# Kernel tuning notes

Measured on AMD Instinct MI355X. Metric: run time of the kernel, lower is better.

Reference implementation:

```python
import jax, jax.numpy as jnp
import numpy as np

E = 1024
H = 16
DH = E // H
FF = 4096
EPS = 1e-5


def setup_inputs() -> dict:
    key = jax.random.key(0)
    ks = jax.random.split(key, 16)
    s = 1.0 / np.sqrt(E)
    sf = 1.0 / np.sqrt(FF)
    inp = {
        'x': jax.random.normal(ks[0], (4, 2048, E), dtype=jnp.float32),
        'Wq': jax.random.uniform(ks[1], (E, E), minval=-s, maxval=s, dtype=jnp.float32),
        'bq': jnp.zeros((E,), jnp.float32),
        'Wk': jax.random.uniform(ks[2], (E, E), minval=-s, maxval=s, dtype=jnp.float32),
        'bk': jnp.zeros((E,), jnp.float32),
        'Wv': jax.random.uniform(ks[3], (E, E), minval=-s, maxval=s, dtype=jnp.float32),
        'bv': jnp.zeros((E,), jnp.float32),
        'Wo': jax.random.uniform(ks[4], (E, E), minval=-s, maxval=s, dtype=jnp.float32),
        'bo': jnp.zeros((E,), jnp.float32),
        'W1': jax.random.uniform(ks[5], (E, FF), minval=-s, maxval=s, dtype=jnp.float32),
        'b1': jnp.zeros((FF,), jnp.float32),
        'W2': jax.random.uniform(ks[6], (FF, E), minval=-sf, maxval=sf, dtype=jnp.float32),
        'b2': jnp.zeros((E,), jnp.float32),
        'g1': jnp.ones((E,), jnp.float32),
        'be1': jnp.zeros((E,), jnp.float32),
        'g2': jnp.ones((E,), jnp.float32),
        'be2': jnp.zeros((E,), jnp.float32),
    }
    return inp


def _layernorm(x, g, b):
    mu = jnp.mean(x, axis=-1, keepdims=True)
    var = jnp.mean(jnp.square(x - mu), axis=-1, keepdims=True)
    return (x - mu) * jax.lax.rsqrt(var + EPS) * g + b


def reference(x, Wq, bq, Wk, bk, Wv, bv, Wo, bo, W1, b1, W2, b2, g1, be1, g2, be2):
    N, S, _ = x.shape
    # project and split heads: (N, H, S, DH)
    def heads(W, b):
        return (x @ W + b).reshape(N, S, H, DH).transpose(0, 2, 1, 3)
    q, k, v = heads(Wq, bq), heads(Wk, bk), heads(Wv, bv)
    scores = jnp.einsum('nhsd,nhtd->nhst', q, k) / np.sqrt(DH)
    attn = jax.nn.softmax(scores, axis=-1)
    ctx = jnp.einsum('nhst,nhtd->nhsd', attn, v)
    ctx = ctx.transpose(0, 2, 1, 3).reshape(N, S, H * DH)
    mh = ctx @ Wo + bo
    norm = _layernorm(mh + x, g1, be1)
    ff = jax.nn.relu(norm @ W1 + b1) @ W2 + b2
    return _layernorm(ff + norm, g2, be2)
```

## Files before the change

### kernel.cpp

```cpp
#include <hip/hip_runtime.h>
#include <hip/hip_bf16.h>
#include <math.h>

#define E_    1024
#define H_    16
#define DH_   64
#define FF_   4096
#define S_    2048
#define NB_   4
#define NTOK_ 8192

typedef float          f32x4_t  __attribute__((ext_vector_type(4)));
typedef unsigned short u16x8_t  __attribute__((ext_vector_type(8)));
typedef unsigned short u16x4_t  __attribute__((ext_vector_type(4)));
typedef __bf16         bf16x8_t __attribute__((ext_vector_type(8)));

#define BC8(x) __builtin_bit_cast(bf16x8_t, (x))

static __device__ __forceinline__ unsigned short f2bf(float f) {
  unsigned u = __float_as_uint(f);
  return (unsigned short)((u + 0x7FFF + ((u >> 16) & 1)) >> 16);
}

static __device__ __forceinline__ void gl16(const unsigned short* g, unsigned short* l) {
  __builtin_amdgcn_global_load_lds((const __attribute__((address_space(1))) void*)g,
                                   (__attribute__((address_space(3))) void*)l, 16, 0, 0);
}

__global__ __launch_bounds__(256)
void cvt_bf16_k(const float* __restrict__ in, unsigned short* __restrict__ out)
{
  const size_t i = ((size_t)blockIdx.x * 256 + threadIdx.x) * 4;
  const float4 v = *(const float4*)&in[i];
  u16x4_t p;
  p[0] = f2bf(v.x); p[1] = f2bf(v.y); p[2] = f2bf(v.z); p[3] = f2bf(v.w);
  *(u16x4_t*)&out[i] = p;
}

__global__ __launch_bounds__(256)
void transpose_bf16_k(const float* __restrict__ W,
                      unsigned short* __restrict__ Th, int K, int N)
{
  __shared__ float tile[64][65];
  const int t  = threadIdx.x;
  const int n0 = blockIdx.x * 64;
  const int k0 = blockIdx.y * 64;
#pragma unroll
  for (int i = 0; i < 4; ++i) {
    const int idx = t + 256 * i;
    const int r  = idx >> 4;
    const int c4 = (idx & 15) * 4;
    const float4 v = *(const float4*)&W[(size_t)(k0 + r) * N + n0 + c4];
    tile[r][c4 + 0] = v.x; tile[r][c4 + 1] = v.y;
    tile[r][c4 + 2] = v.z; tile[r][c4 + 3] = v.w;
  }
  __syncthreads();
#pragma unroll
  for (int i = 0; i < 4; ++i) {
    const int idx = t + 256 * i;
    const int rr  = idx >> 4;
    const int c4  = (idx & 15) * 4;
    u16x4_t hv;
#pragma unroll
    for (int j = 0; j < 4; ++j) hv[j] = f2bf(tile[c4 + j][rr]);
    *(u16x4_t*)&Th[(size_t)(n0 + rr) * K + k0 + c4] = hv;
  }
}

template<int RELU, int MODE>
__global__ __launch_bounds__(256)
void gemm_bf16_k(const unsigned short* __restrict__ A,
                 const unsigned short* __restrict__ Th,
                 const float* __restrict__ bias, void* __restrict__ outp,
                 int M, int N, int K)
{
  __shared__ __align__(16) unsigned short As[128][64];
  __shared__ __align__(16) unsigned short Bs[128][64];
  const int t    = threadIdx.x;
  const int nwg  = gridDim.x * gridDim.y;
  int id = blockIdx.x + gridDim.x * blockIdx.y;
  id = (id & 7) * (nwg >> 3) + (id >> 3);
  const int bn = (id % gridDim.x) * 128;
  const int bm = (id / gridDim.x) * 128;
  const int lane = t & 63;
  const int wid  = t >> 6;
  const int wr   = wid >> 1;
  const int wc   = wid & 1;
  const int fr   = lane & 15;
  const int hi   = lane >> 4;

  const int r8  = lane >> 3;
  const int csw = (lane & 7) ^ r8;

  f32x4_t acc[4][4];
#pragma unroll
  for (int m = 0; m < 4; ++m)
#pragma unroll
    for (int n = 0; n < 4; ++n)
#pragma unroll
      for (int j = 0; j < 4; ++j) acc[m][n][j] = 0.0f;

  const unsigned short* agl = A  + (size_t)(bm + wid * 32 + r8) * K + csw * 8;
  const unsigned short* bgl = Th + (size_t)(bn + wid * 32 + r8) * K + csw * 8;
  unsigned short* al = &As[wid * 32][0];
  unsigned short* bl = &Bs[wid * 32][0];

  for (int k0 = 0; k0 < K; k0 += 64) {
    __syncthreads();
#pragma unroll
    for (int i = 0; i < 4; ++i) {
      gl16(agl + (size_t)(i * 8) * K + k0, al + i * 512);
      gl16(bgl + (size_t)(i * 8) * K + k0, bl + i * 512);
    }
    __syncthreads();
#pragma unroll
    for (int kk = 0; kk < 2; ++kk) {
      u16x8_t aH[4], bH[4];
#pragma unroll
      for (int m = 0; m < 4; ++m)
        aH[m] = *(const u16x8_t*)&As[wr * 64 + m * 16 + fr][(((kk << 2) | hi) ^ (fr & 7)) * 8];
#pragma unroll
      for (int n = 0; n < 4; ++n)
        bH[n] = *(const u16x8_t*)&Bs[wc * 64 + n * 16 + fr][(((kk << 2) | hi) ^ (fr & 7)) * 8];
#pragma unroll
      for (int m = 0; m < 4; ++m)
#pragma unroll
        for (int n = 0; n < 4; ++n)
          acc[m][n] = __builtin_amdgcn_mfma_f32_16x16x32_bf16(BC8(aH[m]), BC8(bH[n]), acc[m][n], 0, 0, 0);
    }
  }

#pragma unroll
  for (int n = 0; n < 4; ++n) {
    const int col = bn + wc * 64 + n * 16 + fr;
    const float bv = bias[col];
#pragma unroll
    for (int m = 0; m < 4; ++m) {
      const int row0 = bm + wr * 64 + m * 16 + hi * 4;
      if (MODE == 2) {
        const int nb = row0 >> 11;
        const int s  = row0 & 2047;
        const int hh = col >> 6;
        const int dd = col & 63;
        u16x4_t pk;
#pragma unroll
        for (int j = 0; j < 4; ++j) pk[j] = f2bf(acc[m][n][j] + bv);
        *(u16x4_t*)&((unsigned short*)outp)[((size_t)((nb * H_ + hh) * DH_ + dd)) * S_ + s] = pk;
      } else {
#pragma unroll
        for (int j = 0; j < 4; ++j) {
          float v = acc[m][n][j] + bv;
          if (RELU) v = fmaxf(v, 0.0f);
          const size_t o = (size_t)(row0 + j) * N + col;
          if (MODE == 0) ((float*)outp)[o] = v;
          else           ((unsigned short*)outp)[o] = f2bf(v);
        }
      }
    }
  }
}

__global__ __launch_bounds__(256)
void attn_mfma_k(const unsigned short* __restrict__ Qg,
                 const unsigned short* __restrict__ Kg,
                 const unsigned short* __restrict__ VTg,
                 unsigned short* __restrict__ Og)
{
  __shared__ __align__(16) unsigned short Ks[64][72];
  __shared__ __align__(16) unsigned short Vt[64][72];
  __shared__ __align__(16) unsigned short Ps[128][72];

  const int t = threadIdx.x;
  const int nwg = gridDim.x * gridDim.y * gridDim.z;
  int id = blockIdx.x + gridDim.x * (blockIdx.y + gridDim.y * blockIdx.z);
  id = (id & 7) * (nwg >> 3) + (id >> 3);
  const int qt = id & 15;
  const int h  = (id >> 4) & 15;
  const int n  = id >> 8;

  const int lane = t & 63;
  const int wid  = t >> 6;
  const int fr   = lane & 15;
  const int hi   = lane >> 4;
  const size_t baseq = (size_t)n * S_ * E_ + (size_t)h * DH_;
  const size_t basev = (size_t)(n * H_ + h) * DH_ * S_;

  u16x8_t qv[2][2];
#pragma unroll
  for (int qf = 0; qf < 2; ++qf)
#pragma unroll
    for (int kk = 0; kk < 2; ++kk)
      qv[qf][kk] = *(const u16x8_t*)&Qg[baseq + (size_t)(qt * 128 + wid * 32 + qf * 16 + fr) * E_ + kk * 32 + hi * 8];

  f32x4_t acc[2][4];
  float m_run[2], l_run[2];
#pragma unroll
  for (int m = 0; m < 2; ++m) {
    m_run[m] = -INFINITY; l_run[m] = 0.0f;
#pragma unroll
    for (int nn = 0; nn < 4; ++nn)
#pragma unroll
      for (int j = 0; j < 4; ++j) acc[m][nn][j] = 0.0f;
  }

  const float cs = 0.18033688011112042f;

  for (int kt = 0; kt < S_ / 64; ++kt) {
    u16x8_t kr[2], vr[2];
#pragma unroll
    for (int i = 0; i < 2; ++i) {
      const int idx = t + 256 * i;
      const int r   = idx >> 3;
      const int c8  = (idx & 7) * 8;
      kr[i] = *(const u16x8_t*)&Kg[baseq + (size_t)(kt * 64 + r) * E_ + c8];
      vr[i] = *(const u16x8_t*)&VTg[basev + (size_t)r * S_ + kt * 64 + c8];
    }
    __syncthreads();
#pragma unroll
    for (int i = 0; i < 2; ++i) {
      const int idx = t + 256 * i;
      const int r   = idx >> 3;
      const int c8  = (idx & 7) * 8;
      *(u16x8_t*)&Ks[r][c8] = kr[i];
      *(u16x8_t*)&Vt[r][c8] = vr[i];
    }
    __syncthreads();

    f32x4_t s[4][2];
#pragma unroll
    for (int kf = 0; kf < 4; ++kf)
#pragma unroll
      for (int qf = 0; qf < 2; ++qf)
#pragma unroll
        for (int j = 0; j < 4; ++j) s[kf][qf][j] = 0.0f;
#pragma unroll
    for (int kk = 0; kk < 2; ++kk) {
      u16x8_t ak[4];
#pragma unroll
      for (int kf = 0; kf < 4; ++kf)
        ak[kf] = *(const u16x8_t*)&Ks[kf * 16 + fr][kk * 32 + hi * 8];
#pragma unroll
      for (int kf = 0; kf < 4; ++kf)
#pragma unroll
        for (int qf = 0; qf < 2; ++qf)
          s[kf][qf] = __builtin_amdgcn_mfma_f32_16x16x32_bf16(BC8(ak[kf]), BC8(qv[qf][kk]), s[kf][qf], 0, 0, 0);
    }

    float corrs[2];
#pragma unroll
    for (int qf = 0; qf < 2; ++qf) {
      float pm = s[0][qf][0];
#pragma unroll
      for (int kf = 0; kf < 4; ++kf)
#pragma unroll
        for (int j = 0; j < 4; ++j) pm = fmaxf(pm, s[kf][qf][j]);
      pm *= cs;
      pm = fmaxf(pm, __shfl_xor(pm, 16));
      pm = fmaxf(pm, __shfl_xor(pm, 32));
      const float mn   = fmaxf(m_run[qf], pm);
      const float corr = exp2f(m_run[qf] - mn);
      float ps = 0.0f;
#pragma unroll
      for (int kf = 0; kf < 4; ++kf)
#pragma unroll
        for (int j = 0; j < 4; ++j) {
          const float pv = exp2f(s[kf][qf][j] * cs - mn);
          Ps[wid * 32 + qf * 16 + fr][kf * 16 + hi * 4 + j] = f2bf(pv);
          ps += pv;
        }
      ps += __shfl_xor(ps, 16);
      ps += __shfl_xor(ps, 32);
      l_run[qf] = l_run[qf] * corr + ps;
      m_run[qf] = mn;
      corrs[qf] = corr;
    }

#pragma unroll
    for (int m = 0; m < 2; ++m)
#pragma unroll
      for (int j = 0; j < 4; ++j) {
        const float ca = __shfl(corrs[m], hi * 20 + j);
#pragma unroll
        for (int nn = 0; nn < 4; ++nn) acc[m][nn][j] *= ca;
      }

    asm volatile("s_waitcnt lgkmcnt(0)" ::: "memory");

#pragma unroll
    for (int kk = 0; kk < 2; ++kk) {
      u16x8_t ap[2], bv[4];
#pragma unroll
      for (int m = 0; m < 2; ++m)
        ap[m] = *(const u16x8_t*)&Ps[wid * 32 + m * 16 + fr][kk * 32 + hi * 8];
#pragma unroll
      for (int nn = 0; nn < 4; ++nn)
        bv[nn] = *(const u16x8_t*)&Vt[nn * 16 + fr][kk * 32 + hi * 8];
#pragma unroll
      for (int m = 0; m < 2; ++m)
#pragma unroll
        for (int nn = 0; nn < 4; ++nn)
          acc[m][nn] = __builtin_amdgcn_mfma_f32_16x16x32_bf16(BC8(ap[m]), BC8(bv[nn]), acc[m][nn], 0, 0, 0);
    }
  }

#pragma unroll
  for (int m = 0; m < 2; ++m)
#pragma unroll
    for (int j = 0; j < 4; ++j) {
      const float inv = 1.0f / __shfl(l_run[m], hi * 20 + j);
      const size_t o = baseq + (size_t)(qt * 128 + wid * 32 + m * 16 + hi * 4 + j) * E_;
#pragma unroll
      for (int nn = 0; nn < 4; ++nn)
        Og[o + nn * 16 + fr] = f2bf(acc[m][nn][j] * inv);
    }
}

template<int WB16>
__global__ __launch_bounds__(256)
void add_ln_k(const float* __restrict__ A, const float* __restrict__ B,
              const float* __restrict__ g, const float* __restrict__ be,
              float* __restrict__ out, unsigned short* __restrict__ outb)
{
  __shared__ float red[8];
  const int row = blockIdx.x;
  const int t = threadIdx.x;
  const size_t off = (size_t)row * E_ + t * 4;
  const float4 a = *(const float4*)&A[off];
  const float4 b = *(const float4*)&B[off];
  float4 x;
  x.x = a.x + b.x; x.y = a.y + b.y; x.z = a.z + b.z; x.w = a.w + b.w;

  float s = x.x + x.y + x.z + x.w;
  s += __shfl_xor(s, 1);  s += __shfl_xor(s, 2);  s += __shfl_xor(s, 4);
  s += __shfl_xor(s, 8);  s += __shfl_xor(s, 16); s += __shfl_xor(s, 32);
  if ((t & 63) == 0) red[t >> 6] = s;
  __syncthreads();
  const float mu = (red[0] + red[1] + red[2] + red[3]) * (1.0f / E_);

  float4 xc;
  xc.x = x.x - mu; xc.y = x.y - mu; xc.z = x.z - mu; xc.w = x.w - mu;
  float q = xc.x*xc.x + xc.y*xc.y + xc.z*xc.z + xc.w*xc.w;
  q += __shfl_xor(q, 1);  q += __shfl_xor(q, 2);  q += __shfl_xor(q, 4);
  q += __shfl_xor(q, 8);  q += __shfl_xor(q, 16); q += __shfl_xor(q, 32);
  __syncthreads();
  if ((t & 63) == 0) red[4 + (t >> 6)] = q;
  __syncthreads();
  const float var = (red[4] + red[5] + red[6] + red[7]) * (1.0f / E_);
  const float inv = rsqrtf(var + 1e-5f);

  const float4 gg = *(const float4*)&g[t * 4];
  const float4 bb = *(const float4*)&be[t * 4];
  float4 o;
  o.x = xc.x * inv * gg.x + bb.x;
  o.y = xc.y * inv * gg.y + bb.y;
  o.z = xc.z * inv * gg.z + bb.z;
  o.w = xc.w * inv * gg.w + bb.w;
  *(float4*)&out[off] = o;
  if (WB16) {
    u16x4_t p;
    p[0] = f2bf(o.x); p[1] = f2bf(o.y); p[2] = f2bf(o.z); p[3] = f2bf(o.w);
    *(u16x4_t*)&outb[off] = p;
  }
}

extern "C" void kernel_launch(void* const* d_in, const int* in_sizes, int n_in,
                              void* d_out, int out_size, void* d_ws, size_t ws_size,
                              hipStream_t stream)
{
  const float* x   = (const float*)d_in[0];
  const float* Wq  = (const float*)d_in[1];
  const float* bq  = (const float*)d_in[2];
  const float* Wk  = (const float*)d_in[3];
  const float* bk  = (const float*)d_in[4];
  const float* Wv  = (const float*)d_in[5];
  const float* bv  = (const float*)d_in[6];
  const float* Wo  = (const float*)d_in[7];
  const float* bo  = (const float*)d_in[8];
  const float* W1  = (const float*)d_in[9];
  const float* b1  = (const float*)d_in[10];
  const float* W2  = (const float*)d_in[11];
  const float* b2  = (const float*)d_in[12];
  const float* g1  = (const float*)d_in[13];
  const float* be1 = (const float*)d_in[14];
  const float* g2  = (const float*)d_in[15];
  const float* be2 = (const float*)d_in[16];
  float* out = (float*)d_out;
  char* wsb  = (char*)d_ws;

  const size_t MB = 1ull << 20;
  unsigned short* xb  = (unsigned short*)(wsb);
  unsigned short* Cb  = (unsigned short*)(wsb);
  unsigned short* Qb  = (unsigned short*)(wsb + 16 * MB);
  unsigned short* Kb  = (unsigned short*)(wsb + 32 * MB);
  unsigned short* F1  = (unsigned short*)(wsb);
  float*          Mh  = (float*)         (wsb + 16 * MB);
  unsigned short* VT  = (unsigned short*)(wsb + 64 * MB);
  float*          N1  = (float*)         (wsb + 80 * MB);
  unsigned short* N1b = (unsigned short*)(wsb + 112 * MB);
  float*          F2  = (float*)         (wsb + 128 * MB);
  unsigned short* ThQ = (unsigned short*)(wsb + 160 * MB);
  unsigned short* ThK = (unsigned short*)(wsb + 162 * MB);
  unsigned short* ThV = (unsigned short*)(wsb + 164 * MB);
  unsigned short* ThO = (unsigned short*)(wsb + 166 * MB);
  unsigned short* Th1 = (unsigned short*)(wsb + 168 * MB);
  unsigned short* Th2 = (unsigned short*)(wsb + 176 * MB);

  dim3 blk(256);
  cvt_bf16_k<<<dim3(NTOK_ * E_ / 1024), blk, 0, stream>>>(x, xb);
  transpose_bf16_k<<<dim3(E_/64,  E_/64),  blk, 0, stream>>>(Wq, ThQ, E_,  E_);
  transpose_bf16_k<<<dim3(E_/64,  E_/64),  blk, 0, stream>>>(Wk, ThK, E_,  E_);
  transpose_bf16_k<<<dim3(E_/64,  E_/64),  blk, 0, stream>>>(Wv, ThV, E_,  E_);
  transpose_bf16_k<<<dim3(E_/64,  E_/64),  blk, 0, stream>>>(Wo, ThO, E_,  E_);
  transpose_bf16_k<<<dim3(FF_/64, E_/64),  blk, 0, stream>>>(W1, Th1, E_,  FF_);
  transpose_bf16_k<<<dim3(E_/64,  FF_/64), blk, 0, stream>>>(W2, Th2, FF_, E_);

  dim3 ge(E_ / 128, NTOK_ / 128);
  dim3 gf(FF_ / 128, NTOK_ / 128);

  gemm_bf16_k<0,1><<<ge, blk, 0, stream>>>(xb,  ThQ, bq, Qb, NTOK_, E_, E_);
  gemm_bf16_k<0,1><<<ge, blk, 0, stream>>>(xb,  ThK, bk, Kb, NTOK_, E_, E_);
  gemm_bf16_k<0,2><<<ge, blk, 0, stream>>>(xb,  ThV, bv, VT, NTOK_, E_, E_);
  attn_mfma_k<<<dim3(S_ / 128, H_, NB_), blk, 0, stream>>>(Qb, Kb, VT, Cb);
  gemm_bf16_k<0,0><<<ge, blk, 0, stream>>>(Cb,  ThO, bo, Mh, NTOK_, E_, E_);
  add_ln_k<1><<<dim3(NTOK_), blk, 0, stream>>>(Mh, x, g1, be1, N1, N1b);
  gemm_bf16_k<1,1><<<gf, blk, 0, stream>>>(N1b, Th1, b1, F1, NTOK_, FF_, E_);
  gemm_bf16_k<0,0><<<ge, blk, 0, stream>>>(F1,  Th2, b2, F2, NTOK_, E_, FF_);
  add_ln_k<0><<<dim3(NTOK_), blk, 0, stream>>>(F2, N1, g2, be2, out, nullptr);
}
```

Before: 606.7 us.

## Fuse QKV projections into one GEMM and add lazy softmax rescaling in attention

The three Q/K/V projection GEMMs become a single GEMM over a concatenated transposed weight of width 3E, with the epilogue routing columns to Q, K, or the transposed V buffer. This removes two launches and improves grid occupancy. In attention, the online-softmax max update and accumulator rescale now run only when some lane's block max exceeds the running max by more than a threshold (8 in log2 units). The P tile is also written with packed bf16 conversion using v_cvt_pk_bf16_f32. The lazy rescale lets probabilities exceed 1 (up to 2^8) before correction, which costs some numerical headroom, and the packed conversion instruction may round differently from the manual f2bf routine.

```diff
diff --git a/kernel.cpp b/kernel.cpp
--- a/kernel.cpp
+++ b/kernel.cpp
@@ -22,6 +22,12 @@
   return (unsigned short)((u + 0x7FFF + ((u >> 16) & 1)) >> 16);
 }
 
+static __device__ __forceinline__ unsigned cvt_pk_bf16(float a, float b) {
+  unsigned r;
+  asm("v_cvt_pk_bf16_f32 %0, %1, %2" : "=v"(r) : "v"(a), "v"(b));
+  return r;
+}
+
 static __device__ __forceinline__ void gl16(const unsigned short* g, unsigned short* l) {
   __builtin_amdgcn_global_load_lds((const __attribute__((address_space(1))) void*)g,
                                    (__attribute__((address_space(3))) void*)l, 16, 0, 0);
@@ -71,7 +77,10 @@
 __global__ __launch_bounds__(256)
 void gemm_bf16_k(const unsigned short* __restrict__ A,
                  const unsigned short* __restrict__ Th,
-                 const float* __restrict__ bias, void* __restrict__ outp,
+                 const float* __restrict__ bias, const float* __restrict__ bias2,
+                 const float* __restrict__ bias3,
+                 void* __restrict__ outp, void* __restrict__ outp2,
+                 void* __restrict__ outp3,
                  int M, int N, int K)
 {
   __shared__ __align__(16) unsigned short As[128][64];
@@ -133,20 +142,30 @@
 #pragma unroll
   for (int n = 0; n < 4; ++n) {
     const int col = bn + wc * 64 + n * 16 + fr;
-    const float bv = bias[col];
 #pragma unroll
     for (int m = 0; m < 4; ++m) {
       const int row0 = bm + wr * 64 + m * 16 + hi * 4;
-      if (MODE == 2) {
-        const int nb = row0 >> 11;
-        const int s  = row0 & 2047;
-        const int hh = col >> 6;
-        const int dd = col & 63;
-        u16x4_t pk;
-#pragma unroll
-        for (int j = 0; j < 4; ++j) pk[j] = f2bf(acc[m][n][j] + bv);
-        *(u16x4_t*)&((unsigned short*)outp)[((size_t)((nb * H_ + hh) * DH_ + dd)) * S_ + s] = pk;
+      if (MODE == 3) {
+        const int sel  = col >> 10;
+        const int colm = col & 1023;
+        const float bv = (sel == 0 ? bias : sel == 1 ? bias2 : bias3)[colm];
+        if (sel == 2) {
+          const int nb = row0 >> 11;
+          const int s  = row0 & 2047;
+          const int hh = colm >> 6;
+          const int dd = colm & 63;
+          u16x4_t pk;
+#pragma unroll
+          for (int j = 0; j < 4; ++j) pk[j] = f2bf(acc[m][n][j] + bv);
+          *(u16x4_t*)&((unsigned short*)outp3)[((size_t)((nb * H_ + hh) * DH_ + dd)) * S_ + s] = pk;
+        } else {
+          unsigned short* dst = (unsigned short*)(sel == 0 ? outp : outp2);
+#pragma unroll
+          for (int j = 0; j < 4; ++j)
+            dst[(size_t)(row0 + j) * 1024 + colm] = f2bf(acc[m][n][j] + bv);
+        }
       } else {
+        const float bv = bias[col];
 #pragma unroll
         for (int j = 0; j < 4; ++j) {
           float v = acc[m][n][j] + bv;
@@ -246,43 +265,59 @@
           s[kf][qf] = __builtin_amdgcn_mfma_f32_16x16x32_bf16(BC8(ak[kf]), BC8(qv[qf][kk]), s[kf][qf], 0, 0, 0);
     }
 
-    float corrs[2];
+    float pml[2];
 #pragma unroll
     for (int qf = 0; qf < 2; ++qf) {
-      float pm = s[0][qf][0];
-#pragma unroll
-      for (int kf = 0; kf < 4; ++kf)
-#pragma unroll
-        for (int j = 0; j < 4; ++j) pm = fmaxf(pm, s[kf][qf][j]);
-      pm *= cs;
-      pm = fmaxf(pm, __shfl_xor(pm, 16));
-      pm = fmaxf(pm, __shfl_xor(pm, 32));
-      const float mn   = fmaxf(m_run[qf], pm);
-      const float corr = exp2f(m_run[qf] - mn);
+      const float a0 = fmaxf(fmaxf(s[0][qf][0], s[0][qf][1]), fmaxf(s[0][qf][2], s[0][qf][3]));
+      const float a1 = fmaxf(fmaxf(s[1][qf][0], s[1][qf][1]), fmaxf(s[1][qf][2], s[1][qf][3]));
+      const float a2 = fmaxf(fmaxf(s[2][qf][0], s[2][qf][1]), fmaxf(s[2][qf][2], s[2][qf][3]));
+      const float a3 = fmaxf(fmaxf(s[3][qf][0], s[3][qf][1]), fmaxf(s[3][qf][2], s[3][qf][3]));
+      pml[qf] = fmaxf(fmaxf(a0, a1), fmaxf(a2, a3)) * cs;
+    }
+
+    const bool need = (pml[0] > m_run[0] + 8.f) || (pml[1] > m_run[1] + 8.f);
+    if (__any(need ? 1 : 0)) {
+      float corr[2];
+#pragma unroll
+      for (int qf = 0; qf < 2; ++qf) {
+        float pm = pml[qf];
+        pm = fmaxf(pm, __shfl_xor(pm, 16));
+        pm = fmaxf(pm, __shfl_xor(pm, 32));
+        const float mn = fmaxf(m_run[qf], pm);
+        corr[qf] = exp2f(m_run[qf] - mn);
+        m_run[qf] = mn;
+        l_run[qf] *= corr[qf];
+      }
+#pragma unroll
+      for (int m = 0; m < 2; ++m)
+#pragma unroll
+        for (int j = 0; j < 4; ++j) {
+          const float ca = __shfl(corr[m], hi * 20 + j);
+#pragma unroll
+          for (int nn = 0; nn < 4; ++nn) acc[m][nn][j] *= ca;
+        }
+    }
+
+#pragma unroll
+    for (int qf = 0; qf < 2; ++qf) {
+      const int prow = wid * 32 + qf * 16 + fr;
       float ps = 0.0f;
 #pragma unroll
-      for (int kf = 0; kf < 4; ++kf)
-#pragma unroll
-        for (int j = 0; j < 4; ++j) {
-          const float pv = exp2f(s[kf][qf][j] * cs - mn);
-          Ps[wid * 32 + qf * 16 + fr][kf * 16 + hi * 4 + j] = f2bf(pv);
-          ps += pv;
-        }
+      for (int kf = 0; kf < 4; ++kf) {
+        const float p0 = exp2f(__builtin_fmaf(s[kf][qf][0], cs, -m_run[qf]));
+        const float p1 = exp2f(__builtin_fmaf(s[kf][qf][1], cs, -m_run[qf]));
+        const float p2 = exp2f(__builtin_fmaf(s[kf][qf][2], cs, -m_run[qf]));
+        const float p3 = exp2f(__builtin_fmaf(s[kf][qf][3], cs, -m_run[qf]));
+        ps += (p0 + p1) + (p2 + p3);
+        uint2 w;
+        w.x = cvt_pk_bf16(p0, p1);
+        w.y = cvt_pk_bf16(p2, p3);
+        *(uint2*)&Ps[prow][kf * 16 + hi * 4] = w;
+      }
       ps += __shfl_xor(ps, 16);
       ps += __shfl_xor(ps, 32);
-      l_run[qf] = l_run[qf] * corr + ps;
-      m_run[qf] = mn;
-      corrs[qf] = corr;
-    }
-
-#pragma unroll
-    for (int m = 0; m < 2; ++m)
-#pragma unroll
-      for (int j = 0; j < 4; ++j) {
-        const float ca = __shfl(corrs[m], hi * 20 + j);
-#pragma unroll
-        for (int nn = 0; nn < 4; ++nn) acc[m][nn][j] *= ca;
-      }
+      l_run[qf] += ps;
+    }
 
     asm volatile("s_waitcnt lgkmcnt(0)" ::: "memory");
 
@@ -398,32 +433,30 @@
   float*          N1  = (float*)         (wsb + 80 * MB);
   unsigned short* N1b = (unsigned short*)(wsb + 112 * MB);
   float*          F2  = (float*)         (wsb + 128 * MB);
-  unsigned short* ThQ = (unsigned short*)(wsb + 160 * MB);
-  unsigned short* ThK = (unsigned short*)(wsb + 162 * MB);
-  unsigned short* ThV = (unsigned short*)(wsb + 164 * MB);
+  unsigned short* ThQKV = (unsigned short*)(wsb + 160 * MB);
+  const size_t EE = (size_t)E_ * E_;
   unsigned short* ThO = (unsigned short*)(wsb + 166 * MB);
   unsigned short* Th1 = (unsigned short*)(wsb + 168 * MB);
   unsigned short* Th2 = (unsigned short*)(wsb + 176 * MB);
 
   dim3 blk(256);
   cvt_bf16_k<<<dim3(NTOK_ * E_ / 1024), blk, 0, stream>>>(x, xb);
-  transpose_bf16_k<<<dim3(E_/64,  E_/64),  blk, 0, stream>>>(Wq, ThQ, E_,  E_);
-  transpose_bf16_k<<<dim3(E_/64,  E_/64),  blk, 0, stream>>>(Wk, ThK, E_,  E_);
-  transpose_bf16_k<<<dim3(E_/64,  E_/64),  blk, 0, stream>>>(Wv, ThV, E_,  E_);
+  transpose_bf16_k<<<dim3(E_/64,  E_/64),  blk, 0, stream>>>(Wq, ThQKV,          E_,  E_);
+  transpose_bf16_k<<<dim3(E_/64,  E_/64),  blk, 0, stream>>>(Wk, ThQKV + EE,     E_,  E_);
+  transpose_bf16_k<<<dim3(E_/64,  E_/64),  blk, 0, stream>>>(Wv, ThQKV + 2 * EE, E_,  E_);
   transpose_bf16_k<<<dim3(E_/64,  E_/64),  blk, 0, stream>>>(Wo, ThO, E_,  E_);
   transpose_bf16_k<<<dim3(FF_/64, E_/64),  blk, 0, stream>>>(W1, Th1, E_,  FF_);
   transpose_bf16_k<<<dim3(E_/64,  FF_/64), blk, 0, stream>>>(W2, Th2, FF_, E_);
 
-  dim3 ge(E_ / 128, NTOK_ / 128);
-  dim3 gf(FF_ / 128, NTOK_ / 128);
-
-  gemm_bf16_k<0,1><<<ge, blk, 0, stream>>>(xb,  ThQ, bq, Qb, NTOK_, E_, E_);
-  gemm_bf16_k<0,1><<<ge, blk, 0, stream>>>(xb,  ThK, bk, Kb, NTOK_, E_, E_);
-  gemm_bf16_k<0,2><<<ge, blk, 0, stream>>>(xb,  ThV, bv, VT, NTOK_, E_, E_);
+  dim3 ge (E_ / 128,      NTOK_ / 128);
+  dim3 ge3(3 * E_ / 128,  NTOK_ / 128);
+  dim3 gf (FF_ / 128,     NTOK_ / 128);
+
+  gemm_bf16_k<0,3><<<ge3, blk, 0, stream>>>(xb, ThQKV, bq, bk, bv, Qb, Kb, VT, NTOK_, 3 * E_, E_);
   attn_mfma_k<<<dim3(S_ / 128, H_, NB_), blk, 0, stream>>>(Qb, Kb, VT, Cb);
-  gemm_bf16_k<0,0><<<ge, blk, 0, stream>>>(Cb,  ThO, bo, Mh, NTOK_, E_, E_);
+  gemm_bf16_k<0,0><<<ge, blk, 0, stream>>>(Cb, ThO, bo, nullptr, nullptr, Mh, nullptr, nullptr, NTOK_, E_, E_);
   add_ln_k<1><<<dim3(NTOK_), blk, 0, stream>>>(Mh, x, g1, be1, N1, N1b);
-  gemm_bf16_k<1,1><<<gf, blk, 0, stream>>>(N1b, Th1, b1, F1, NTOK_, FF_, E_);
-  gemm_bf16_k<0,0><<<ge, blk, 0, stream>>>(F1,  Th2, b2, F2, NTOK_, E_, FF_);
+  gemm_bf16_k<1,1><<<gf, blk, 0, stream>>>(N1b, Th1, b1, nullptr, nullptr, F1, nullptr, nullptr, NTOK_, FF_, E_);
+  gemm_bf16_k<0,0><<<ge, blk, 0, stream>>>(F1, Th2, b2, nullptr, nullptr, F2, nullptr, nullptr, NTOK_, E_, FF_);
   add_ln_k<0><<<dim3(NTOK_), blk, 0, stream>>>(F2, N1, g2, be2, out, nullptr);
 }
```

New measurement: 603.4 us. No clear change (-0.6%).
